# Performance work log

Measured on AMD Instinct MI355X. Metric: run time of the kernel, lower is better.

## Reference

```python
import jax, jax.numpy as jnp
import numpy as np
from jax import lax

HEIGHT, WIDTH = 13, 10
HIDDEN = 256
CONV_OUT = 32 * 3 * 2  # 192, matches torch _get_conv_output_size


def setup_inputs() -> dict:
    key = jax.random.key(0)
    ks = jax.random.split(key, 12)
    B, T = 128, 512
    s = 0.05
    return {
        "x": jax.random.normal(ks[0], (B, T, HEIGHT, WIDTH), jnp.float32),
        "conv1_w": jax.random.normal(ks[1], (16, 1, 3, 3), jnp.float32) * s,
        "conv1_b": jax.random.normal(ks[2], (16,), jnp.float32) * s,
        "conv2_w": jax.random.normal(ks[3], (32, 16, 3, 3), jnp.float32) * s,
        "conv2_b": jax.random.normal(ks[4], (32,), jnp.float32) * s,
        "W_ih": jax.random.normal(ks[5], (4 * HIDDEN, CONV_OUT), jnp.float32) * s,
        "b_ih": jax.random.normal(ks[6], (4 * HIDDEN,), jnp.float32) * s,
        "W_hh": jax.random.normal(ks[7], (4 * HIDDEN, HIDDEN), jnp.float32) * s,
        "b_hh": jax.random.normal(ks[8], (4 * HIDDEN,), jnp.float32) * s,
        "cls_w": jax.random.normal(ks[9], (64, HIDDEN), jnp.float32) * s,
        "cls_b": jax.random.normal(ks[10], (64,), jnp.float32) * s,
    }


def _conv2d(x, w, b):
    # NCHW, OIHW, padding=1 (SAME for 3x3)
    y = lax.conv_general_dilated(x, w, window_strides=(1, 1),
                                 padding=((1, 1), (1, 1)),
                                 dimension_numbers=("NCHW", "OIHW", "NCHW"))
    return y + b[None, :, None, None]


def _maxpool2(x):
    # kernel 2, stride 2, VALID (floor) like nn.MaxPool2d(2)
    return lax.reduce_window(x, -jnp.inf, lax.max,
                             (1, 1, 2, 2), (1, 1, 2, 2), "VALID")


def reference(x, conv1_w, conv1_b, conv2_w, conv2_b, W_ih, b_ih, W_hh, b_hh, cls_w, cls_b):
    B, T, Hd, Wd = x.shape
    xi = x.reshape(B * T, 1, Hd, Wd)
    y = _maxpool2(jax.nn.relu(_conv2d(xi, conv1_w, conv1_b)))
    y = _maxpool2(jax.nn.relu(_conv2d(y, conv2_w, conv2_b)))
    feat = y.reshape(B, T, -1)  # [B, T, 192], channel-major flatten matches torch view

    # Precompute input contribution to gates for all steps (same math, batched)
    gx_all = jnp.einsum("btf,gf->btg", feat, W_ih) + b_ih + b_hh  # [B, T, 4H]
    H = W_hh.shape[1]

    def step(carry, gx):
        h, c = carry
        gates = gx + h @ W_hh.T  # [B, 4H]
        i, f, g, o = jnp.split(gates, 4, axis=1)
        i = jax.nn.sigmoid(i)
        f = jax.nn.sigmoid(f)
        g = jnp.tanh(g)
        o = jax.nn.sigmoid(o)
        c = f * c + i * g
        h = o * jnp.tanh(c)
        return (h, c), None

    h0 = jnp.zeros((B, H), x.dtype)
    c0 = jnp.zeros((B, H), x.dtype)
    (hT, _), _ = lax.scan(step, (h0, c0), jnp.swapaxes(gx_all, 0, 1))
    logits = hT @ cls_w.T + cls_b
    return logits
```

## Files before the change

### kernel.cpp

```cpp
#include <hip/hip_runtime.h>
#include <hip/hip_bf16.h>


typedef _Float16 half2v __attribute__((ext_vector_type(2)));
typedef _Float16 f16x8 __attribute__((ext_vector_type(8)));
typedef float f32x4 __attribute__((ext_vector_type(4)));

__device__ __forceinline__ float dot2f16(half2v a, half2v b, float c) {
#if defined(__has_builtin)
#if __has_builtin(__builtin_amdgcn_fdot2)
    return __builtin_amdgcn_fdot2(a, b, c, false);
#else
    return c + (float)a.x * (float)b.x + (float)a.y * (float)b.y;
#endif
#else
    return c + (float)a.x * (float)b.x + (float)a.y * (float)b.y;
#endif
}

__device__ __forceinline__ unsigned int packf2(const float* p) {
    half2v hv;
    hv.x = (_Float16)p[0];
    hv.y = (_Float16)p[1];
    return __builtin_bit_cast(unsigned int, hv);
}

__device__ __forceinline__ half2v bch2(unsigned int u) {
    return __builtin_bit_cast(half2v, u);
}

__device__ __forceinline__ uint4 pack8(const float* p) {
    uint4 v;
    v.x = packf2(p + 0);
    v.y = packf2(p + 2);
    v.z = packf2(p + 4);
    v.w = packf2(p + 6);
    return v;
}

__global__ __launch_bounds__(256) void prepack_w_kernel(
    const float* __restrict__ Wih, uint4* __restrict__ wf)
{
    int idx = blockIdx.x * 256 + threadIdx.x;
    if (idx < 1024 * 192 / 8) wf[idx] = pack8(Wih + idx * 8);
}

__global__ __launch_bounds__(256) void prepack_sw_kernel(
    const float* __restrict__ Whh, uint4* __restrict__ sw)
{
    int idx = blockIdx.x * 256 + threadIdx.x;
    if (idx < 13 * 1024) {
        int c = idx >> 10, r = idx & 1023;
        sw[idx] = pack8(Whh + (size_t)r * 256 + 152 + 8 * c);
    }
}

__global__ __launch_bounds__(256) void conv_kernel(
    const float* __restrict__ x,
    const float* __restrict__ c1w,
    const float* __restrict__ c1b,
    const float* __restrict__ c2w,
    const float* __restrict__ c2b,
    _Float16* __restrict__ feat)
{
    __shared__ float w1t[9 * 16];
    __shared__ float b1s[16];
    __shared__ float w2t[16 * 9 * 32];
    __shared__ float b2s[32];
    __shared__ float xp[4][14 * 12];
    __shared__ float p1p[4][16 * 8 * 7];

    const int tid = threadIdx.x;

    for (int idx = tid; idx < 144; idx += 256) {
        int oc = idx / 9, k = idx % 9;
        w1t[k * 16 + oc] = c1w[idx];
    }
    if (tid < 16) b1s[tid] = c1b[tid];
    for (int idx = tid; idx < 4608; idx += 256) {
        int oc = idx / 144, ic = (idx / 9) % 16, k = idx % 9;
        w2t[(ic * 9 + k) * 32 + oc] = c2w[idx];
    }
    if (tid < 32) b2s[tid] = c2b[tid];

    const int w = tid >> 6;
    const int lane = tid & 63;
    const int img = blockIdx.x * 4 + w;

    for (int i = lane; i < 14 * 12; i += 64) xp[w][i] = 0.f;
    for (int i = lane; i < 16 * 8 * 7; i += 64) p1p[w][i] = 0.f;
    __syncthreads();

    const float* xin = x + (size_t)img * 130;
    for (int i = lane; i < 130; i += 64) {
        int r = i / 10, c = i % 10;
        xp[w][(r + 1) * 12 + (c + 1)] = xin[i];
    }
    __syncthreads();

    {
        const int oc = lane & 15, q = lane >> 4;
        #pragma unroll
        for (int i = 0; i < 8; i++) {
            int pos = i * 4 + q;
            if (pos < 30) {
                int ph = pos / 5, pw = pos % 5;
                float cmax = -1e30f;
                #pragma unroll
                for (int pt = 0; pt < 4; pt++) {
                    int Y = 2 * ph + (pt >> 1), X = 2 * pw + (pt & 1);
                    float s = 0.f;
                    #pragma unroll
                    for (int k = 0; k < 9; k++) {
                        int dy = k / 3, dx = k % 3;
                        s += w1t[k * 16 + oc] * xp[w][(Y + dy) * 12 + X + dx];
                    }
                    cmax = fmaxf(cmax, s);
                }
                p1p[w][(oc * 8 + ph + 1) * 7 + (pw + 1)] = fmaxf(0.f, cmax + b1s[oc]);
            }
        }
    }
    __syncthreads();

    {
        const int oc = lane & 31, pw2 = lane >> 5;
        float acc[3][4];
        #pragma unroll
        for (int a = 0; a < 3; a++)
            #pragma unroll
            for (int b = 0; b < 4; b++) acc[a][b] = 0.f;

        for (int ic = 0; ic < 16; ic++) {
            #pragma unroll
            for (int k = 0; k < 9; k++) {
                int dy = k / 3, dx = k % 3;
                float wv = w2t[(ic * 9 + k) * 32 + oc];
                #pragma unroll
                for (int ph2 = 0; ph2 < 3; ph2++) {
                    #pragma unroll
                    for (int pt = 0; pt < 4; pt++) {
                        int y = 2 * ph2 + (pt >> 1) + dy;
                        int xx = 2 * pw2 + (pt & 1) + dx;
                        acc[ph2][pt] += wv * p1p[w][(ic * 8 + y) * 7 + xx];
                    }
                }
            }
        }
        float bias = b2s[oc];
        _Float16* fo = feat + (size_t)img * 192;
        #pragma unroll
        for (int ph2 = 0; ph2 < 3; ph2++) {
            float m = fmaxf(fmaxf(acc[ph2][0], acc[ph2][1]),
                            fmaxf(acc[ph2][2], acc[ph2][3]));
            fo[oc * 6 + ph2 * 2 + pw2] = (_Float16)fmaxf(0.f, m + bias);
        }
    }
}

__global__ __launch_bounds__(256, 1) void gemm_gx_kernel(
    const _Float16* __restrict__ feat,
    const _Float16* __restrict__ wf16,
    const float* __restrict__ bih,
    const float* __restrict__ bhh,
    _Float16* __restrict__ gx)
{
    __shared__ uint4 As4[128][25];
    __shared__ uint4 Ws4[128][25];

    const int tid = threadIdx.x;
    const int n0 = blockIdx.x * 128;
    const int m0 = blockIdx.y * 128;

    #pragma unroll
    for (int it = 0; it < 12; it++) {
        int q = tid + it * 256;
        int r = q / 24, c = q % 24;
        As4[r][c] = *(const uint4*)(feat + (size_t)(m0 + r) * 192 + c * 8);
        Ws4[r][c] = *(const uint4*)(wf16 + (size_t)(n0 + r) * 192 + c * 8);
    }
    __syncthreads();

    const int w = tid >> 6;
    const int lane = tid & 63;
    const int lm = lane & 15;
    const int lk = lane >> 4;

    f32x4 acc[2][8] = {};
    #pragma unroll
    for (int ks = 0; ks < 6; ks++) {
        f16x8 wf[2], af[8];
        #pragma unroll
        for (int nf = 0; nf < 2; nf++)
            wf[nf] = __builtin_bit_cast(f16x8, Ws4[w * 32 + nf * 16 + lm][ks * 4 + lk]);
        #pragma unroll
        for (int mf = 0; mf < 8; mf++)
            af[mf] = __builtin_bit_cast(f16x8, As4[mf * 16 + lm][ks * 4 + lk]);
        #pragma unroll
        for (int nf = 0; nf < 2; nf++)
            #pragma unroll
            for (int mf = 0; mf < 8; mf++)
                acc[nf][mf] = __builtin_amdgcn_mfma_f32_16x16x32_f16(
                    wf[nf], af[mf], acc[nf][mf], 0, 0, 0);
    }

    #pragma unroll
    for (int nf = 0; nf < 2; nf++) {
        int nb = n0 + w * 32 + nf * 16 + lk * 4;
        float4 b1 = *(const float4*)&bih[nb];
        float4 b2 = *(const float4*)&bhh[nb];
        float bs0 = b1.x + b2.x, bs1 = b1.y + b2.y;
        float bs2 = b1.z + b2.z, bs3 = b1.w + b2.w;
        #pragma unroll
        for (int mf = 0; mf < 8; mf++) {
            int m = m0 + mf * 16 + lm;
            union { _Float16 h[4]; uint2 u; } pk;
            pk.h[0] = (_Float16)(acc[nf][mf][0] + bs0);
            pk.h[1] = (_Float16)(acc[nf][mf][1] + bs1);
            pk.h[2] = (_Float16)(acc[nf][mf][2] + bs2);
            pk.h[3] = (_Float16)(acc[nf][mf][3] + bs3);
            *(uint2*)&gx[(size_t)m * 1024 + nb] = pk.u;
        }
    }
}

__global__ __launch_bounds__(512, 2) void lstm_kernel(
    const _Float16* __restrict__ gx,
    const float* __restrict__ Whh,
    const uint4* __restrict__ sw,
    const float* __restrict__ clsw,
    const float* __restrict__ clsb,
    float* __restrict__ out)
{
    __shared__ uint4 wl4[9][1024];
    __shared__ __align__(16) _Float16 hbuf[2][256];
    __shared__ float xg[512];

    const int t = threadIdx.x;
    const int b = blockIdx.x;
    const int r0 = t, r1 = t + 512;

    const float* w0 = Whh + (size_t)r0 * 256;
    const float* w1 = Whh + (size_t)r1 * 256;

    #pragma unroll
    for (int ch = 0; ch < 9; ch++) {
        wl4[ch][r0] = pack8(w0 + 8 * ch);
        wl4[ch][r1] = pack8(w1 + 8 * ch);
    }
    half2v wr0[40], wr1[40];
    #pragma unroll
    for (int q = 0; q < 40; q++) {
        wr0[q] = bch2(packf2(w0 + 72 + 2 * q));
        wr1[q] = bch2(packf2(w1 + 72 + 2 * q));
    }
    if (t < 256) hbuf[0][t] = (_Float16)0.f;
    __syncthreads();

    float c = 0.f;
    int cur = 0;
    const _Float16* gxb = gx + (size_t)b * 512 * 1024;
    float ga = (float)gxb[r0];
    float gb = (float)gxb[r1];

    for (int step = 0; step < 512; step++) {
        const _Float16* gxn = gxb + (size_t)((step + 1) & 511) * 1024;
        _Float16 na = gxn[r0];
        _Float16 nb = gxn[r1];

        float acc0 = ga, acc1 = gb;
        const uint4* hb4 = (const uint4*)&hbuf[cur][0];

        #pragma unroll
        for (int sc = 0; sc < 13; sc++) {
            uint4 u0 = sw[sc * 1024 + r0];
            uint4 u1 = sw[sc * 1024 + r1];
            uint4 hv = hb4[19 + sc];
            acc0 = dot2f16(bch2(u0.x), bch2(hv.x), acc0);
            acc0 = dot2f16(bch2(u0.y), bch2(hv.y), acc0);
            acc0 = dot2f16(bch2(u0.z), bch2(hv.z), acc0);
            acc0 = dot2f16(bch2(u0.w), bch2(hv.w), acc0);
            acc1 = dot2f16(bch2(u1.x), bch2(hv.x), acc1);
            acc1 = dot2f16(bch2(u1.y), bch2(hv.y), acc1);
            acc1 = dot2f16(bch2(u1.z), bch2(hv.z), acc1);
            acc1 = dot2f16(bch2(u1.w), bch2(hv.w), acc1);
        }
        #pragma unroll
        for (int ch = 0; ch < 9; ch++) {
            uint4 u0 = wl4[ch][r0];
            uint4 u1 = wl4[ch][r1];
            uint4 hv = hb4[ch];
            acc0 = dot2f16(bch2(u0.x), bch2(hv.x), acc0);
            acc0 = dot2f16(bch2(u0.y), bch2(hv.y), acc0);
            acc0 = dot2f16(bch2(u0.z), bch2(hv.z), acc0);
            acc0 = dot2f16(bch2(u0.w), bch2(hv.w), acc0);
            acc1 = dot2f16(bch2(u1.x), bch2(hv.x), acc1);
            acc1 = dot2f16(bch2(u1.y), bch2(hv.y), acc1);
            acc1 = dot2f16(bch2(u1.z), bch2(hv.z), acc1);
            acc1 = dot2f16(bch2(u1.w), bch2(hv.w), acc1);
        }
        #pragma unroll
        for (int cc = 0; cc < 10; cc++) {
            uint4 hv = hb4[9 + cc];
            acc0 = dot2f16(wr0[4 * cc + 0], bch2(hv.x), acc0);
            acc0 = dot2f16(wr0[4 * cc + 1], bch2(hv.y), acc0);
            acc0 = dot2f16(wr0[4 * cc + 2], bch2(hv.z), acc0);
            acc0 = dot2f16(wr0[4 * cc + 3], bch2(hv.w), acc0);
            acc1 = dot2f16(wr1[4 * cc + 0], bch2(hv.x), acc1);
            acc1 = dot2f16(wr1[4 * cc + 1], bch2(hv.y), acc1);
            acc1 = dot2f16(wr1[4 * cc + 2], bch2(hv.z), acc1);
            acc1 = dot2f16(wr1[4 * cc + 3], bch2(hv.w), acc1);
        }

        if (t >= 256) {
            xg[t - 256] = acc0;
            xg[t] = acc1;
        }
        __syncthreads();
        if (t < 256) {
            float i_ = 1.f / (1.f + __expf(-acc0));
            float g_ = 1.f - 2.f / (__expf(2.f * acc1) + 1.f);
            float f_ = 1.f / (1.f + __expf(-xg[t]));
            float o_ = 1.f / (1.f + __expf(-xg[t + 256]));
            c = f_ * c + i_ * g_;
            float th = 1.f - 2.f / (__expf(2.f * c) + 1.f);
            float h = o_ * th;
            hbuf[cur ^ 1][t] = (_Float16)h;
        }
        __syncthreads();
        cur ^= 1;
        ga = (float)na;
        gb = (float)nb;
    }

    if (t < 64) {
        const float* cw = clsw + t * 256;
        float s = clsb[t];
        for (int k = 0; k < 256; k++) s += cw[k] * (float)hbuf[cur][k];
        out[b * 64 + t] = s;
    }
}

extern "C" void kernel_launch(void* const* d_in, const int* in_sizes, int n_in,
                              void* d_out, int out_size, void* d_ws, size_t ws_size,
                              hipStream_t stream) {
    const float* x    = (const float*)d_in[0];
    const float* c1w  = (const float*)d_in[1];
    const float* c1b  = (const float*)d_in[2];
    const float* c2w  = (const float*)d_in[3];
    const float* c2b  = (const float*)d_in[4];
    const float* Wih  = (const float*)d_in[5];
    const float* bih  = (const float*)d_in[6];
    const float* Whh  = (const float*)d_in[7];
    const float* bhh  = (const float*)d_in[8];
    const float* clsw = (const float*)d_in[9];
    const float* clsb = (const float*)d_in[10];

    _Float16* feat = (_Float16*)d_ws;
    _Float16* gx   = feat + (size_t)65536 * 192;
    uint4* aux     = (uint4*)(gx + (size_t)65536 * 1024);
    float* outp = (float*)d_out;

    hipLaunchKernelGGL(prepack_w_kernel, dim3(96), dim3(256), 0, stream, Wih, aux);
    hipLaunchKernelGGL(conv_kernel, dim3(16384), dim3(256), 0, stream,
                       x, c1w, c1b, c2w, c2b, feat);
    hipLaunchKernelGGL(gemm_gx_kernel, dim3(8, 512), dim3(256), 0, stream,
                       feat, (const _Float16*)aux, bih, bhh, gx);
    hipLaunchKernelGGL(prepack_sw_kernel, dim3(52), dim3(256), 0, stream, Whh, aux);
    hipLaunchKernelGGL(lstm_kernel, dim3(128), dim3(512), 0, stream,
                       gx, Whh, aux, clsw, clsb, outp);
}
```

Measured before the change: 1.293 ms.

## Use fp16 dot2 for conv2 and rebalance LSTM weight split across LDS/registers/global

Conv2 now stores pooled conv1 activations and conv2 weights as packed fp16 pairs in channel-interleaved shared memory. It accumulates with fdot2, caching an 8x4 input patch per channel pair in registers, which halves the multiply count and the LDS traffic. The LSTM recurrent matvec moves 4 more columns of W_hh out of the global-streamed chunk: 2 columns into a new LDS uint2 array and 2 more into registers, shrinking per-step global/L2 weight loads. This raises register pressure (84 half2 regs per thread) and lowers conv precision to fp16 inputs.

```diff
diff --git a/kernel.cpp b/kernel.cpp
--- a/kernel.cpp
+++ b/kernel.cpp
@@ -18,10 +18,21 @@
 #endif
 }
 
+__device__ __forceinline__ float dot2u(unsigned int a, unsigned int b, float c) {
+    return dot2f16(__builtin_bit_cast(half2v, a), __builtin_bit_cast(half2v, b), c);
+}
+
 __device__ __forceinline__ unsigned int packf2(const float* p) {
     half2v hv;
     hv.x = (_Float16)p[0];
     hv.y = (_Float16)p[1];
+    return __builtin_bit_cast(unsigned int, hv);
+}
+
+__device__ __forceinline__ unsigned int packff(float a, float b) {
+    half2v hv;
+    hv.x = (_Float16)a;
+    hv.y = (_Float16)b;
     return __builtin_bit_cast(unsigned int, hv);
 }
 
@@ -49,9 +60,9 @@
     const float* __restrict__ Whh, uint4* __restrict__ sw)
 {
     int idx = blockIdx.x * 256 + threadIdx.x;
-    if (idx < 13 * 1024) {
+    if (idx < 12 * 1024) {
         int c = idx >> 10, r = idx & 1023;
-        sw[idx] = pack8(Whh + (size_t)r * 256 + 152 + 8 * c);
+        sw[idx] = pack8(Whh + (size_t)r * 256 + 160 + 8 * c);
     }
 }
 
@@ -65,10 +76,10 @@
 {
     __shared__ float w1t[9 * 16];
     __shared__ float b1s[16];
-    __shared__ float w2t[16 * 9 * 32];
+    __shared__ unsigned int w2h[8 * 9 * 32];
     __shared__ float b2s[32];
     __shared__ float xp[4][14 * 12];
-    __shared__ float p1p[4][16 * 8 * 7];
+    __shared__ __align__(4) _Float16 p1ph[4][8 * 7 * 16];
 
     const int tid = threadIdx.x;
 
@@ -77,9 +88,12 @@
         w1t[k * 16 + oc] = c1w[idx];
     }
     if (tid < 16) b1s[tid] = c1b[tid];
-    for (int idx = tid; idx < 4608; idx += 256) {
-        int oc = idx / 144, ic = (idx / 9) % 16, k = idx % 9;
-        w2t[(ic * 9 + k) * 32 + oc] = c2w[idx];
+    for (int idx = tid; idx < 2304; idx += 256) {
+        int icp = idx / 288, rem = idx % 288;
+        int k = rem / 32, oc = rem % 32;
+        float a = c2w[oc * 144 + (2 * icp) * 9 + k];
+        float b = c2w[oc * 144 + (2 * icp + 1) * 9 + k];
+        w2h[idx] = packff(a, b);
     }
     if (tid < 32) b2s[tid] = c2b[tid];
 
@@ -88,7 +102,7 @@
     const int img = blockIdx.x * 4 + w;
 
     for (int i = lane; i < 14 * 12; i += 64) xp[w][i] = 0.f;
-    for (int i = lane; i < 16 * 8 * 7; i += 64) p1p[w][i] = 0.f;
+    for (int i = lane; i < 8 * 7 * 16; i += 64) p1ph[w][i] = (_Float16)0.f;
     __syncthreads();
 
     const float* xin = x + (size_t)img * 130;
@@ -117,7 +131,8 @@
                     }
                     cmax = fmaxf(cmax, s);
                 }
-                p1p[w][(oc * 8 + ph + 1) * 7 + (pw + 1)] = fmaxf(0.f, cmax + b1s[oc]);
+                p1ph[w][((ph + 1) * 7 + (pw + 1)) * 16 + oc] =
+                    (_Float16)fmaxf(0.f, cmax + b1s[oc]);
             }
         }
     }
@@ -125,24 +140,31 @@
 
     {
         const int oc = lane & 31, pw2 = lane >> 5;
-        float acc[3][4];
-        #pragma unroll
-        for (int a = 0; a < 3; a++)
+        float acc[3][4] = {};
+        const _Float16* P = &p1ph[w][0];
+
+        #pragma unroll
+        for (int icp = 0; icp < 8; icp++) {
+            unsigned int hreg[32];
             #pragma unroll
-            for (int b = 0; b < 4; b++) acc[a][b] = 0.f;
-
-        for (int ic = 0; ic < 16; ic++) {
+            for (int y = 0; y < 8; y++)
+                #pragma unroll
+                for (int xx = 0; xx < 4; xx++) {
+                    int xcol = 2 * pw2 + xx;
+                    hreg[y * 4 + xx] =
+                        *(const unsigned int*)&P[(y * 7 + xcol) * 16 + 2 * icp];
+                }
             #pragma unroll
             for (int k = 0; k < 9; k++) {
                 int dy = k / 3, dx = k % 3;
-                float wv = w2t[(ic * 9 + k) * 32 + oc];
+                unsigned int wv = w2h[(icp * 9 + k) * 32 + oc];
                 #pragma unroll
                 for (int ph2 = 0; ph2 < 3; ph2++) {
                     #pragma unroll
                     for (int pt = 0; pt < 4; pt++) {
                         int y = 2 * ph2 + (pt >> 1) + dy;
-                        int xx = 2 * pw2 + (pt & 1) + dx;
-                        acc[ph2][pt] += wv * p1p[w][(ic * 8 + y) * 7 + xx];
+                        int xx2 = (pt & 1) + dx;
+                        acc[ph2][pt] = dot2u(wv, hreg[y * 4 + xx2], acc[ph2][pt]);
                     }
                 }
             }
@@ -233,6 +255,7 @@
     float* __restrict__ out)
 {
     __shared__ uint4 wl4[9][1024];
+    __shared__ uint2 wl2[1024];
     __shared__ __align__(16) _Float16 hbuf[2][256];
     __shared__ float xg[512];
 
@@ -248,11 +271,18 @@
         wl4[ch][r0] = pack8(w0 + 8 * ch);
         wl4[ch][r1] = pack8(w1 + 8 * ch);
     }
-    half2v wr0[40], wr1[40];
+    {
+        uint2 v0, v1;
+        v0.x = packf2(w0 + 72); v0.y = packf2(w0 + 74);
+        v1.x = packf2(w1 + 72); v1.y = packf2(w1 + 74);
+        wl2[r0] = v0;
+        wl2[r1] = v1;
+    }
+    half2v wr0[42], wr1[42];
     #pragma unroll
-    for (int q = 0; q < 40; q++) {
-        wr0[q] = bch2(packf2(w0 + 72 + 2 * q));
-        wr1[q] = bch2(packf2(w1 + 72 + 2 * q));
+    for (int q = 0; q < 42; q++) {
+        wr0[q] = bch2(packf2(w0 + 76 + 2 * q));
+        wr1[q] = bch2(packf2(w1 + 76 + 2 * q));
     }
     if (t < 256) hbuf[0][t] = (_Float16)0.f;
     __syncthreads();
@@ -272,10 +302,10 @@
         const uint4* hb4 = (const uint4*)&hbuf[cur][0];
 
         #pragma unroll
-        for (int sc = 0; sc < 13; sc++) {
+        for (int sc = 0; sc < 12; sc++) {
             uint4 u0 = sw[sc * 1024 + r0];
             uint4 u1 = sw[sc * 1024 + r1];
-            uint4 hv = hb4[19 + sc];
+            uint4 hv = hb4[20 + sc];
             acc0 = dot2f16(bch2(u0.x), bch2(hv.x), acc0);
             acc0 = dot2f16(bch2(u0.y), bch2(hv.y), acc0);
             acc0 = dot2f16(bch2(u0.z), bch2(hv.z), acc0);
@@ -299,17 +329,30 @@
             acc1 = dot2f16(bch2(u1.z), bch2(hv.z), acc1);
             acc1 = dot2f16(bch2(u1.w), bch2(hv.w), acc1);
         }
+        {
+            uint4 hv = hb4[9];
+            uint2 u0 = wl2[r0];
+            uint2 u1 = wl2[r1];
+            acc0 = dot2f16(bch2(u0.x), bch2(hv.x), acc0);
+            acc0 = dot2f16(bch2(u0.y), bch2(hv.y), acc0);
+            acc1 = dot2f16(bch2(u1.x), bch2(hv.x), acc1);
+            acc1 = dot2f16(bch2(u1.y), bch2(hv.y), acc1);
+            acc0 = dot2f16(wr0[0], bch2(hv.z), acc0);
+            acc0 = dot2f16(wr0[1], bch2(hv.w), acc0);
+            acc1 = dot2f16(wr1[0], bch2(hv.z), acc1);
+            acc1 = dot2f16(wr1[1], bch2(hv.w), acc1);
+        }
         #pragma unroll
         for (int cc = 0; cc < 10; cc++) {
-            uint4 hv = hb4[9 + cc];
-            acc0 = dot2f16(wr0[4 * cc + 0], bch2(hv.x), acc0);
-            acc0 = dot2f16(wr0[4 * cc + 1], bch2(hv.y), acc0);
-            acc0 = dot2f16(wr0[4 * cc + 2], bch2(hv.z), acc0);
-            acc0 = dot2f16(wr0[4 * cc + 3], bch2(hv.w), acc0);
-            acc1 = dot2f16(wr1[4 * cc + 0], bch2(hv.x), acc1);
-            acc1 = dot2f16(wr1[4 * cc + 1], bch2(hv.y), acc1);
-            acc1 = dot2f16(wr1[4 * cc + 2], bch2(hv.z), acc1);
-            acc1 = dot2f16(wr1[4 * cc + 3], bch2(hv.w), acc1);
+            uint4 hv = hb4[10 + cc];
+            acc0 = dot2f16(wr0[2 + 4 * cc + 0], bch2(hv.x), acc0);
+            acc0 = dot2f16(wr0[2 + 4 * cc + 1], bch2(hv.y), acc0);
+            acc0 = dot2f16(wr0[2 + 4 * cc + 2], bch2(hv.z), acc0);
+            acc0 = dot2f16(wr0[2 + 4 * cc + 3], bch2(hv.w), acc0);
+            acc1 = dot2f16(wr1[2 + 4 * cc + 0], bch2(hv.x), acc1);
+            acc1 = dot2f16(wr1[2 + 4 * cc + 1], bch2(hv.y), acc1);
+            acc1 = dot2f16(wr1[2 + 4 * cc + 2], bch2(hv.z), acc1);
+            acc1 = dot2f16(wr1[2 + 4 * cc + 3], bch2(hv.w), acc1);
         }
 
         if (t >= 256) {
@@ -366,7 +409,7 @@
                        x, c1w, c1b, c2w, c2b, feat);
     hipLaunchKernelGGL(gemm_gx_kernel, dim3(8, 512), dim3(256), 0, stream,
                        feat, (const _Float16*)aux, bih, bhh, gx);
-    hipLaunchKernelGGL(prepack_sw_kernel, dim3(52), dim3(256), 0, stream, Whh, aux);
+    hipLaunchKernelGGL(prepack_sw_kernel, dim3(48), dim3(256), 0, stream, Whh, aux);
     hipLaunchKernelGGL(lstm_kernel, dim3(128), dim3(512), 0, stream,
                        gx, Whh, aux, clsw, clsb, outp);
 }
```

Measured after the change: 1.105 ms. 14.5% less time.
